# Kernel tuning notes

Measured on AMD Instinct MI355X. Metric: run time of the kernel, lower is better.

## Reference

```python
import jax, jax.numpy as jnp
import numpy as np
import math

N = 1000000          # num_primitives
G = 512              # grid_size
M = 64               # max_elements_per_cell
RES = 512
FOCAL = RES / 2.0 / (0.5 / 1.5)   # 768.0, from e = 1.5/0.5
K = 2                # candidate cells per axis (ellipses are tiny: radius ~1e-3)
PRIM_TYPE = 5.0      # _ROTATED_ELLIPSE_PRIM_TYPE


def _build_mvp(seed=42):
    rng = np.random.default_rng(seed)
    x, n, f = 0.5, 1.5, 100.0
    proj = np.array([[n / x, 0, 0, 0], [0, -n / x, 0, 0],
                     [0, 0, -(f + n) / (f - n), -(2 * f * n) / (f - n)],
                     [0, 0, -1, 0]], dtype=np.float32)
    u1, u2, u3 = rng.random(3)
    qx = math.sqrt(1 - u1) * math.sin(math.tau * u2)
    qy = math.sqrt(1 - u1) * math.cos(math.tau * u2)
    qz = math.sqrt(u1) * math.sin(math.tau * u3)
    qw = math.sqrt(u1) * math.cos(math.tau * u3)
    rot = np.eye(4, dtype=np.float32)
    rot[:3, :3] = np.array(
        [[1 - 2 * (qy * qy + qz * qz), 2 * (qx * qy - qz * qw), 2 * (qx * qz + qy * qw)],
         [2 * (qx * qy + qz * qw), 1 - 2 * (qx * qx + qz * qz), 2 * (qy * qz - qx * qw)],
         [2 * (qx * qz - qy * qw), 2 * (qy * qz + qx * qw), 1 - 2 * (qx * qx + qy * qy)]],
        dtype=np.float32)
    trans = np.eye(4, dtype=np.float32)
    trans[2, 3] = -4.0
    return proj @ (trans @ rot)


def setup_inputs() -> dict:
    key = jax.random.key(0)
    k = jax.random.split(key, 4)
    centers = (jax.random.uniform(k[0], (N, 3)) - 0.5) / 0.5
    scales = 1e-3 * jax.random.uniform(k[1], (N, 3))
    rotations = jnp.ones((N, 4), jnp.float32)
    colors = jax.random.uniform(k[2], (N, 3))
    opacities = jax.random.uniform(k[3], (N,))
    mvp = jnp.asarray(_build_mvp())
    background = jnp.zeros((3,), jnp.float32)
    return {"centers": centers, "scales": scales, "rotations": rotations,
            "colors": colors, "opacities": opacities, "mvp": mvp,
            "background": background}


def _quat_to_rot(q):
    q = q / jnp.clip(jnp.linalg.norm(q, axis=1, keepdims=True), 1e-12, None)
    w, x, y, z = q[:, 0], q[:, 1], q[:, 2], q[:, 3]
    return jnp.stack([
        1 - 2 * (y * y + z * z), 2 * (x * y - z * w), 2 * (x * z + y * w),
        2 * (x * y + z * w), 1 - 2 * (x * x + z * z), 2 * (y * z - x * w),
        2 * (x * z - y * w), 2 * (y * z + x * w), 1 - 2 * (x * x + y * y)],
        axis=-1).reshape(-1, 3, 3)


def reference(centers, scales, rotations, colors, opacities, mvp, background):
    dt = centers.dtype
    # --- project centers to NDC (no perspective divide, per source) ---
    ndc = jnp.concatenate([centers, jnp.ones((N, 1), dt)], axis=1) @ mvp.T  # [N,4]
    valid = ndc[:, 2] > 0.0
    cs = (ndc[:, :2] + 1.0) * 0.5                                          # [N,2] in [0,1]
    # --- 3D covariance -> screen-space 2x2 covariance ---
    Rm = _quat_to_rot(rotations)
    L = Rm * jnp.clip(scales, 1e-9, None)[:, None, :]   # R @ diag(s)
    cov = jnp.einsum('nij,nkj->nik', L, L)              # L L^T
    V = mvp[:3, :3]
    ccov = jnp.einsum('ij,njk,lk->nil', V, cov, V)      # V cov V^T
    z = jnp.clip(ndc[:, 2], 1e-6, None)
    sc = FOCAL / z
    scov = ccov[:, :2, :2] * (sc * sc)[:, None, None]
    # --- depth sort (invalid prims pushed to the back, kept for static shape) ---
    order = jnp.argsort(jnp.where(valid, z, jnp.float32(1e30)))
    cs, scov = cs[order], scov[order]
    col = colors[order]
    op = jnp.clip(opacities, 0.0, 1.0)[order]
    vm = valid[order]
    vf = vm.astype(dt)
    cx, cy = cs[:, 0], cs[:, 1]
    c00, c01, c11 = scov[:, 0, 0], scov[:, 0, 1], scov[:, 1, 1]
    # --- packed param block: 20 floats per primitive ---
    cp = jnp.stack([cx, cy, c00, c01, c11, jnp.zeros_like(cx)], axis=1) * vf[:, None]
    result = jnp.concatenate([
        (PRIM_TYPE * vf)[:, None],            # slot 0: prim type
        cp,                                   # slots 1..6: control points
        jnp.zeros((N, 2), dt),                # slots 7,8
        col * vf[:, None],                    # slots 9..11: color
        (op * vf)[:, None],                   # slot 12: opacity
        jnp.zeros((N, 7), dt)], axis=1)       # slots 13..19
    # --- acceleration grid: scatter depth-sorted prim ids into covered cells ---
    rx = 3.0 * jnp.sqrt(jnp.clip(c00, 0.0, None)) / RES   # 3-sigma extent, normalized
    ry = 3.0 * jnp.sqrt(jnp.clip(c11, 0.0, None)) / RES
    x0 = jnp.floor((cx - rx) * G).astype(jnp.int32)
    x1 = jnp.floor((cx + rx) * G).astype(jnp.int32)
    y0 = jnp.floor((cy - ry) * G).astype(jnp.int32)
    y1 = jnp.floor((cy + ry) * G).astype(jnp.int32)
    offs = jnp.arange(K, dtype=jnp.int32)
    cxc = x0[:, None] + offs
    cyc = y0[:, None] + offs
    vx = (cxc <= x1[:, None]) & (cxc >= 0) & (cxc < G)
    vy = (cyc <= y1[:, None]) & (cyc >= 0) & (cyc < G)
    cell = cyc[:, :, None] * G + cxc[:, None, :]                     # [N,K,K]
    vp = vm[:, None, None] & vy[:, :, None] & vx[:, None, :]
    key_arr = jnp.where(vp, cell, G * G).reshape(-1)                 # sentinel G*G
    prim = jnp.broadcast_to(jnp.arange(N, dtype=jnp.int32)[:, None, None], (N, K, K)).reshape(-1)
    ordr = jnp.argsort(key_arr)                                      # stable sort by cell
    sk = key_arr[ordr]
    sp = prim[ordr]
    first = jnp.searchsorted(sk, sk, side='left').astype(jnp.int32)
    rank = jnp.arange(sk.shape[0], dtype=jnp.int32) - first
    ok = (sk < G * G) & (rank < M)
    slots = jnp.where(ok, sk * (M + 1) + 1 + rank, G * G * (M + 1))
    grid = jnp.zeros(G * G * (M + 1), jnp.int32).at[slots].set(sp, mode='drop')
    counts = jax.ops.segment_sum((sk < G * G).astype(jnp.int32), sk, num_segments=G * G + 1)[:G * G]
    grid = grid.at[jnp.arange(G * G) * (M + 1)].set(jnp.minimum(counts, M))
    header = jnp.concatenate([vm.sum().astype(dt)[None],
                              jnp.array([float(G), float(M)], dt)])
    return jnp.concatenate([header, background, result.reshape(-1), grid.astype(dt)])
```

## Files before the change

### kernel.cpp

```cpp
#include <hip/hip_runtime.h>
#include <stdint.h>

#pragma clang fp contract(off)

#define N_PRIM   1000000
#define GRID_G   512
#define NCELLS   (GRID_G*GRID_G)
#define FOCAL_C  768.0f
#define NP2      1048576
#define SB       1024
#define EPB      1024
#define PREP_BLOCKS 2048

#define O_SORTA  ((size_t)0)
#define O_SORTB  (O_SORTA + (size_t)NP2*8)
#define O_REC    (O_SORTB + (size_t)NP2*8)
#define O_CCNT   (O_REC   + (size_t)N_PRIM*64)
#define O_COFS   (O_CCNT  + (size_t)NCELLS*4)
#define O_CURS   (O_COFS  + (size_t)NCELLS*4)
#define O_HIST   (O_CURS  + (size_t)NCELLS*4)
#define O_BSUM   (O_HIST  + (size_t)NCELLS*4)
#define O_VCNT   (O_BSUM  + 8192)
#define O_ENTRY  (O_VCNT  + 8192)
#define WS_NEED  (O_ENTRY + (size_t)4*N_PRIM*4)

__device__ __forceinline__ int swz(int q) { return q ^ ((q >> 3) & 7); }

__global__ __launch_bounds__(256) void k_prep(
    const float* __restrict__ centers, const float* __restrict__ scales,
    const float* __restrict__ rotations, const float* __restrict__ colors,
    const float* __restrict__ opac, const float* __restrict__ mvp,
    uint64_t* __restrict__ sortA, float4* __restrict__ rec,
    uint32_t* __restrict__ cellcnt, uint32_t* __restrict__ vcnt)
{
  __shared__ float4 srec[2048];
  __shared__ uint32_t swcnt[4];
  int t = threadIdx.x;
  int pair = blockIdx.x*256 + t;
  int p0 = pair*2;
  bool live = p0 < N_PRIM;

  float m0=mvp[0], m1=mvp[1], m2=mvp[2],  m3=mvp[3];
  float m4=mvp[4], m5=mvp[5], m6=mvp[6],  m7=mvp[7];
  float m8=mvp[8], m9=mvp[9], m10=mvp[10],m11=mvp[11];

  bool valid0=false, valid1=false;
  uint64_t pk0 = ~0ULL, pk1 = ~0ULL;

  if (live) {
    const float2* cp = (const float2*)(centers + (size_t)pair*6);
    float2 ca = cp[0], cb = cp[1], cc = cp[2];
    const float2* sp = (const float2*)(scales + (size_t)pair*6);
    float2 sa = sp[0], sb2 = sp[1], sc2 = sp[2];
    const float4* rp = (const float4*)rotations;
    float4 q0 = rp[p0], q1 = rp[p0+1];
    const float2* colp = (const float2*)(colors + (size_t)pair*6);
    float2 ka = colp[0], kb = colp[1], kc = colp[2];
    float2 o2 = ((const float2*)opac)[pair];

    auto doPrim = [&](int i, float c0, float c1, float c2,
                      float s0, float s1, float s2,
                      float qw, float qx, float qy, float qz,
                      float col0, float col1, float col2, float op,
                      uint64_t& pk, bool& validf, int lidx) {
      float n0 = fmaf(m2,  c2, fmaf(m1, c1, m0*c0)) + m3;
      float n1 = fmaf(m6,  c2, fmaf(m5, c1, m4*c0)) + m7;
      float n2 = fmaf(m10, c2, fmaf(m9, c1, m8*c0)) + m11;
      bool valid = n2 > 0.0f;
      validf = valid;
      float cx = (n0 + 1.0f)*0.5f;
      float cy = (n1 + 1.0f)*0.5f;
      uint32_t key32 = valid ? __float_as_uint(fmaxf(n2, 1e-6f)) : 0x7149F2CAu;
      pk = ((uint64_t)key32 << 20) | (uint32_t)i;

      float nrm = sqrtf(qw*qw + qx*qx + qy*qy + qz*qz);
      nrm = fmaxf(nrm, 1e-12f);
      qw /= nrm; qx /= nrm; qy /= nrm; qz /= nrm;
      float R00 = 1.0f - 2.0f*(qy*qy + qz*qz);
      float R01 = 2.0f*(qx*qy - qz*qw);
      float R02 = 2.0f*(qx*qz + qy*qw);
      float R10 = 2.0f*(qx*qy + qz*qw);
      float R11 = 1.0f - 2.0f*(qx*qx + qz*qz);
      float R12 = 2.0f*(qy*qz - qx*qw);
      float R20 = 2.0f*(qx*qz - qy*qw);
      float R21 = 2.0f*(qy*qz + qx*qw);
      float R22 = 1.0f - 2.0f*(qx*qx + qy*qy);
      s0 = fmaxf(s0, 1e-9f); s1 = fmaxf(s1, 1e-9f); s2 = fmaxf(s2, 1e-9f);
      float L00=R00*s0, L01=R01*s1, L02=R02*s2;
      float L10=R10*s0, L11=R11*s1, L12=R12*s2;
      float L20=R20*s0, L21=R21*s1, L22=R22*s2;
      float cv00 = fmaf(L02,L02, fmaf(L01,L01, L00*L00));
      float cv01 = fmaf(L02,L12, fmaf(L01,L11, L00*L10));
      float cv02 = fmaf(L02,L22, fmaf(L01,L21, L00*L20));
      float cv11 = fmaf(L12,L12, fmaf(L11,L11, L10*L10));
      float cv12 = fmaf(L12,L22, fmaf(L11,L21, L10*L20));
      float cv22 = fmaf(L22,L22, fmaf(L21,L21, L20*L20));
      float T00 = fmaf(m2,cv02, fmaf(m1,cv01, m0*cv00));
      float T01 = fmaf(m2,cv12, fmaf(m1,cv11, m0*cv01));
      float T02 = fmaf(m2,cv22, fmaf(m1,cv12, m0*cv02));
      float T10 = fmaf(m6,cv02, fmaf(m5,cv01, m4*cv00));
      float T11 = fmaf(m6,cv12, fmaf(m5,cv11, m4*cv01));
      float T12 = fmaf(m6,cv22, fmaf(m5,cv12, m4*cv02));
      float cc00 = fmaf(T02,m2, fmaf(T01,m1, T00*m0));
      float cc01 = fmaf(T02,m6, fmaf(T01,m5, T00*m4));
      float cc11 = fmaf(T12,m6, fmaf(T11,m5, T10*m4));
      float zc  = fmaxf(n2, 1e-6f);
      float scv = FOCAL_C / zc;
      float sc22 = scv*scv;
      float c00 = cc00*sc22, c01 = cc01*sc22, c11 = cc11*sc22;

      float rx = (3.0f * sqrtf(fmaxf(c00, 0.0f))) / 512.0f;
      float ry = (3.0f * sqrtf(fmaxf(c11, 0.0f))) / 512.0f;
      int x0 = (int)floorf((cx - rx) * 512.0f);
      int x1 = (int)floorf((cx + rx) * 512.0f);
      int y0 = (int)floorf((cy - ry) * 512.0f);
      int y1 = (int)floorf((cy + ry) * 512.0f);
      int cl[4];
      #pragma unroll
      for (int ky = 0; ky < 2; ++ky) {
        int yy = y0 + ky;
        bool vy = (yy <= y1) && (yy >= 0) && (yy < GRID_G);
        #pragma unroll
        for (int kx = 0; kx < 2; ++kx) {
          int xx = x0 + kx;
          bool vx = (xx <= x1) && (xx >= 0) && (xx < GRID_G);
          int cell = (valid && vy && vx) ? (yy*GRID_G + xx) : -1;
          cl[ky*2+kx] = cell;
          if (cell >= 0) atomicAdd(&cellcnt[cell], 1u);
        }
      }
      float opv = fminf(fmaxf(op, 0.0f), 1.0f);
      float vf = valid ? 1.0f : 0.0f;
      int lb = lidx*4;
      srec[swz(lb+0)] = make_float4(cx, cy, c00, c01);
      srec[swz(lb+1)] = make_float4(c11, col0, col1, col2);
      srec[swz(lb+2)] = make_float4(opv, vf, 0.0f, 0.0f);
      srec[swz(lb+3)] = make_float4(__int_as_float(cl[0]), __int_as_float(cl[1]),
                                    __int_as_float(cl[2]), __int_as_float(cl[3]));
    };

    doPrim(p0,   ca.x, ca.y, cb.x, sa.x, sa.y, sb2.x,
           q0.x, q0.y, q0.z, q0.w, ka.x, ka.y, kb.x, o2.x, pk0, valid0, 2*t);
    doPrim(p0+1, cb.y, cc.x, cc.y, sb2.y, sc2.x, sc2.y,
           q1.x, q1.y, q1.z, q1.w, kb.y, kc.x, kc.y, o2.y, pk1, valid1, 2*t+1);
  }

  ((ulonglong2*)sortA)[pair] = make_ulonglong2(pk0, pk1);

  unsigned long long b0 = __ballot(live && valid0);
  unsigned long long b1 = __ballot(live && valid1);
  if ((t & 63) == 0) swcnt[t >> 6] = (uint32_t)(__popcll(b0) + __popcll(b1));
  __syncthreads();
  if (t == 0) vcnt[blockIdx.x] = swcnt[0]+swcnt[1]+swcnt[2]+swcnt[3];

  size_t gbase = (size_t)blockIdx.x*2048;
  for (int q = t; q < 2048; q += 256) {
    size_t gi = gbase + q;
    if (gi < (size_t)N_PRIM*4) rec[gi] = srec[swz(q)];
  }
}

__global__ void k_scanA(const uint32_t* __restrict__ cnt, uint32_t* __restrict__ ofs,
                        uint32_t* __restrict__ bsum)
{
  __shared__ uint32_t s[256];
  int t = threadIdx.x;
  int i = blockIdx.x*256 + t;
  uint32_t v = cnt[i];
  s[t] = v; __syncthreads();
  for (int o = 1; o < 256; o <<= 1) {
    uint32_t u = (t >= o) ? s[t-o] : 0u; __syncthreads();
    s[t] += u; __syncthreads();
  }
  ofs[i] = s[t] - v;
  if (t == 255) bsum[blockIdx.x] = s[t];
}

__global__ void k_scanBC(uint32_t* __restrict__ ofs, const uint32_t* __restrict__ bsum,
                         uint32_t* __restrict__ cursor,
                         const uint32_t* __restrict__ vcnt,
                         const float* __restrict__ bg, float* __restrict__ out)
{
  __shared__ uint32_t s[256];
  int t = threadIdx.x;
  int bid = blockIdx.x;
  uint32_t acc = 0;
  for (int i = t; i < bid; i += 256) acc += bsum[i];
  s[t] = acc; __syncthreads();
  #pragma unroll
  for (int o = 128; o > 0; o >>= 1) { if (t < o) s[t] += s[t+o]; __syncthreads(); }
  uint32_t partial = s[0];
  int i = bid*256 + t;
  uint32_t v = ofs[i] + partial;
  ofs[i] = v;
  if (cursor) cursor[i] = v;

  if (vcnt && bid == 0) {
    __syncthreads();
    uint32_t a2 = 0;
    for (int i2 = t; i2 < PREP_BLOCKS; i2 += 256) a2 += vcnt[i2];
    s[t] = a2; __syncthreads();
    #pragma unroll
    for (int o = 128; o > 0; o >>= 1) { if (t < o) s[t] += s[t+o]; __syncthreads(); }
    if (t == 0) {
      out[0] = (float)s[0];
      out[1] = 512.0f;
      out[2] = 64.0f;
      out[3] = bg[0]; out[4] = bg[1]; out[5] = bg[2];
    }
  }
}

__global__ __launch_bounds__(256) void k_hist(const uint64_t* __restrict__ keys,
                                              uint32_t* __restrict__ hist, int shift)
{
  __shared__ uint32_t h[256];
  int t = threadIdx.x;
  h[t] = 0; __syncthreads();
  const ulonglong2* k2 = (const ulonglong2*)(keys + (size_t)blockIdx.x*EPB);
  #pragma unroll
  for (int j = 0; j < 2; ++j) {
    ulonglong2 w = k2[j*256 + t];
    atomicAdd(&h[(uint32_t)(w.x >> shift) & 255u], 1u);
    atomicAdd(&h[(uint32_t)(w.y >> shift) & 255u], 1u);
  }
  __syncthreads();
  hist[(size_t)t*SB + blockIdx.x] = h[t];
}

__global__ __launch_bounds__(256) void k_scatter(
    const uint64_t* __restrict__ in, uint64_t* __restrict__ outp,
    const uint32_t* __restrict__ hist, int shift)
{
  __shared__ uint32_t s_base[256];
  __shared__ uint32_t lbase[256];
  __shared__ uint32_t s_run[256];
  __shared__ uint32_t s_wcnt[1024];
  __shared__ uint64_t stage[EPB];
  int t = threadIdx.x;
  int wid = t >> 6, lane = t & 63;
  s_base[t] = hist[(size_t)t*SB + blockIdx.x];
  s_run[t] = 0;
  lbase[t] = 0;
  size_t base = (size_t)blockIdx.x*EPB;
  uint64_t v[4]; uint32_t d[4];
  #pragma unroll
  for (int j = 0; j < 4; ++j) {
    v[j] = in[base + j*256 + t];
    d[j] = (uint32_t)(v[j] >> shift) & 255u;
  }
  __syncthreads();
  #pragma unroll
  for (int j = 0; j < 4; ++j) atomicAdd(&lbase[d[j]], 1u);
  __syncthreads();
  uint32_t mycnt = lbase[t];
  for (int o = 1; o < 256; o <<= 1) {
    uint32_t u = (t >= o) ? lbase[t-o] : 0u; __syncthreads();
    lbase[t] += u; __syncthreads();
  }
  uint32_t myexcl = lbase[t] - mycnt;
  __syncthreads();
  lbase[t] = myexcl;
  __syncthreads();

  #pragma unroll
  for (int j = 0; j < 4; ++j) {
    #pragma unroll
    for (int q0 = 0; q0 < 4; ++q0) s_wcnt[q0*256 + t] = 0;
    __syncthreads();
    unsigned long long m = ~0ULL;
    #pragma unroll
    for (int bit = 0; bit < 8; ++bit) {
      unsigned long long vote = __ballot((d[j] >> bit) & 1);
      m &= ((d[j] >> bit) & 1) ? vote : ~vote;
    }
    uint32_t lr = __popcll(m & ((1ULL << lane) - 1ULL));
    if (lr == 0) s_wcnt[d[j]*4 + wid] = (uint32_t)__popcll(m);
    __syncthreads();
    uint32_t wb = 0;
    #pragma unroll
    for (int w = 0; w < 3; ++w) if (w < wid) wb += s_wcnt[d[j]*4 + w];
    stage[lbase[d[j]] + s_run[d[j]] + wb + lr] = v[j];
    __syncthreads();
    s_run[t] += s_wcnt[t*4] + s_wcnt[t*4+1] + s_wcnt[t*4+2] + s_wcnt[t*4+3];
    __syncthreads();
  }
  #pragma unroll
  for (int j = 0; j < 4; ++j) {
    int q = j*256 + t;
    uint64_t sv = stage[q];
    uint32_t sd = (uint32_t)(sv >> shift) & 255u;
    outp[s_base[sd] + ((uint32_t)q - lbase[sd])] = sv;
  }
}

__global__ __launch_bounds__(256) void k_result(
    const uint64_t* __restrict__ sorted, const float4* __restrict__ rec,
    uint32_t* __restrict__ cursor, uint32_t* __restrict__ entry,
    float* __restrict__ out)
{
  __shared__ float rows[64*21];
  int t = threadIdx.x;
  int i = blockIdx.x*256 + t;
  bool liveP = i < N_PRIM;
  float4 a = make_float4(0,0,0,0), b = a, c = a;
  int4 cl = make_int4(-1,-1,-1,-1);
  if (liveP) {
    uint64_t v = sorted[i];
    int o = (int)(v & 0xFFFFFu);
    a = rec[(size_t)o*4]; b = rec[(size_t)o*4+1];
    c = rec[(size_t)o*4+2];
    float4 dd = rec[(size_t)o*4+3];
    cl.x = __float_as_int(dd.x); cl.y = __float_as_int(dd.y);
    cl.z = __float_as_int(dd.z); cl.w = __float_as_int(dd.w);
  }
  float vf = c.y;
  int mychunk = t >> 6;
  int r64 = t & 63;
  int blockRows = min(256, N_PRIM - blockIdx.x*256);
  for (int ch = 0; ch < 4; ++ch) {
    if (mychunk == ch && liveP) {
      float* r = &rows[r64*21];
      r[0]  = 5.0f*vf;
      r[1]  = a.x*vf; r[2] = a.y*vf; r[3] = a.z*vf; r[4] = a.w*vf; r[5] = b.x*vf;
      r[6]  = 0.0f; r[7] = 0.0f; r[8] = 0.0f;
      r[9]  = b.y*vf; r[10] = b.z*vf; r[11] = b.w*vf;
      r[12] = c.x*vf;
      r[13]=0.0f; r[14]=0.0f; r[15]=0.0f; r[16]=0.0f; r[17]=0.0f; r[18]=0.0f; r[19]=0.0f;
    }
    __syncthreads();
    int nrows = min(64, blockRows - ch*64);
    if (nrows > 0) {
      int total = nrows*20;
      float* gout = out + 6 + (size_t)blockIdx.x*5120 + ch*1280;
      for (int g = t; g < total; g += 256) {
        int rr = g/20, cc2 = g - rr*20;
        gout[g] = rows[rr*21+cc2];
      }
    }
    __syncthreads();
  }
  if (liveP) {
    int cc[4] = {cl.x, cl.y, cl.z, cl.w};
    #pragma unroll
    for (int k = 0; k < 4; ++k) {
      if (cc[k] >= 0) {
        uint32_t p = atomicAdd(&cursor[cc[k]], 1u);
        entry[p] = (uint32_t)i;
      }
    }
  }
}

__global__ __launch_bounds__(256) void k_grid(
    const uint32_t* __restrict__ cellcnt, const uint32_t* __restrict__ cellofs,
    const uint32_t* __restrict__ entry, float* __restrict__ out)
{
  int wid = threadIdx.x >> 6;
  int lane = threadIdx.x & 63;
  int cell = blockIdx.x*4 + wid;
  uint32_t cnt = cellcnt[cell];
  uint32_t ofs = cellofs[cell];
  float* g = out + 6 + (size_t)N_PRIM*20 + (size_t)cell*65;
  if (cnt <= 64u) {
    int v = (lane < (int)cnt) ? (int)entry[ofs + lane] : 0x7FFFFFFF;
    #pragma unroll
    for (int k = 2; k <= 64; k <<= 1) {
      #pragma unroll
      for (int j = k>>1; j > 0; j >>= 1) {
        int p = __shfl_xor(v, j, 64);
        bool up = ((lane & k) == 0);
        bool lower = ((lane & j) == 0);
        int mn = min(v,p), mx = max(v,p);
        v = (up == lower) ? mn : mx;
      }
    }
    g[1+lane] = (lane < (int)cnt) ? (float)v : 0.0f;
    if (lane == 0) g[0] = (float)cnt;
  } else {
    int last = -1;
    for (int s = 0; s < 64; ++s) {
      int best = 0x7FFFFFFF;
      for (uint32_t c = lane; c < cnt; c += 64) {
        int v = (int)entry[ofs + c];
        if (v > last && v < best) best = v;
      }
      #pragma unroll
      for (int o = 32; o > 0; o >>= 1) best = min(best, __shfl_xor(best, o, 64));
      if (lane == 0) g[1+s] = (float)best;
      last = best;
    }
    if (lane == 0) g[0] = 64.0f;
  }
}

extern "C" void kernel_launch(void* const* d_in, const int* in_sizes, int n_in,
                              void* d_out, int out_size, void* d_ws, size_t ws_size,
                              hipStream_t stream)
{
  const float* centers   = (const float*)d_in[0];
  const float* scales    = (const float*)d_in[1];
  const float* rotations = (const float*)d_in[2];
  const float* colors    = (const float*)d_in[3];
  const float* opacities = (const float*)d_in[4];
  const float* mvp       = (const float*)d_in[5];
  const float* background= (const float*)d_in[6];
  float* out = (float*)d_out;
  char* ws = (char*)d_ws;
  if (ws_size < WS_NEED) return;

  uint64_t* sortA  = (uint64_t*)(ws + O_SORTA);
  uint64_t* sortB  = (uint64_t*)(ws + O_SORTB);
  float4*   rec    = (float4*)  (ws + O_REC);
  uint32_t* ccnt   = (uint32_t*)(ws + O_CCNT);
  uint32_t* cofs   = (uint32_t*)(ws + O_COFS);
  uint32_t* curs   = (uint32_t*)(ws + O_CURS);
  uint32_t* hist   = (uint32_t*)(ws + O_HIST);
  uint32_t* bsum   = (uint32_t*)(ws + O_BSUM);
  uint32_t* vcnt   = (uint32_t*)(ws + O_VCNT);
  uint32_t* entry  = (uint32_t*)(ws + O_ENTRY);

  hipMemsetAsync(ws + O_CCNT, 0, (size_t)NCELLS*4, stream);

  k_prep<<<PREP_BLOCKS, 256, 0, stream>>>(centers, scales, rotations, colors,
                                          opacities, mvp, sortA, rec, ccnt, vcnt);

  k_scanA <<<NCELLS/256, 256, 0, stream>>>(ccnt, cofs, bsum);
  k_scanBC<<<NCELLS/256, 256, 0, stream>>>(cofs, bsum, curs, vcnt, background, out);

  uint64_t *kin = sortA, *kout = sortB;
  const int shifts[4] = {20, 28, 36, 44};
  for (int pass = 0; pass < 4; ++pass) {
    k_hist<<<SB, 256, 0, stream>>>(kin, hist, shifts[pass]);
    k_scanA <<<(256*SB)/256, 256, 0, stream>>>(hist, hist, bsum);
    k_scanBC<<<(256*SB)/256, 256, 0, stream>>>(hist, bsum, (uint32_t*)nullptr,
                                               (const uint32_t*)nullptr,
                                               (const float*)nullptr, (float*)nullptr);
    k_scatter<<<SB, 256, 0, stream>>>(kin, kout, hist, shifts[pass]);
    uint64_t* tmp = kin; kin = kout; kout = tmp;
  }

  k_result<<<(N_PRIM+255)/256, 256, 0, stream>>>(kin, rec, curs, entry, out);
  k_grid  <<<NCELLS/4, 256, 0, stream>>>(ccnt, cofs, entry, out);
}
```

Measured before the change: 423.3 us.

## Replace 4-pass radix sort with depth-bucket counting sort and in-bucket rank

Drops the four-pass LSD radix sort over 64-bit keys. Each valid primitive's depth bits are offset by a constant and binned into 262144 buckets; the bucket counts are scanned together with the cell counts in one fused scan. Items are then scattered into their buckets, and each bucket is ordered by an O(n^2) rank count inside one wavefront, which writes the output rows and grid entries directly. Unused tail rows are zeroed separately. This saves many kernel launches and global passes, but relies on the depth distribution fitting the chosen key range and on buckets staying small.

```diff
diff --git a/kernel.cpp b/kernel.cpp
--- a/kernel.cpp
+++ b/kernel.cpp
@@ -4,24 +4,24 @@
 #pragma clang fp contract(off)
 
 #define N_PRIM   1000000
+#define NPAIRS   (N_PRIM/2)
+#define PREP_BLOCKS ((NPAIRS+255)/256)
 #define GRID_G   512
 #define NCELLS   (GRID_G*GRID_G)
+#define NBUCK    262144
 #define FOCAL_C  768.0f
-#define NP2      1048576
-#define SB       1024
-#define EPB      1024
-#define PREP_BLOCKS 2048
-
-#define O_SORTA  ((size_t)0)
-#define O_SORTB  (O_SORTA + (size_t)NP2*8)
-#define O_REC    (O_SORTB + (size_t)NP2*8)
-#define O_CCNT   (O_REC   + (size_t)N_PRIM*64)
-#define O_COFS   (O_CCNT  + (size_t)NCELLS*4)
-#define O_CURS   (O_COFS  + (size_t)NCELLS*4)
-#define O_HIST   (O_CURS  + (size_t)NCELLS*4)
-#define O_BSUM   (O_HIST  + (size_t)NCELLS*4)
-#define O_VCNT   (O_BSUM  + 8192)
-#define O_ENTRY  (O_VCNT  + 8192)
+#define KEYC     0x358637BDu
+
+#define O_PK     ((size_t)0)
+#define O_REC    (O_PK   + (size_t)N_PRIM*8)
+#define O_BSLOT  (O_REC  + (size_t)N_PRIM*64)
+#define O_CNT    (O_BSLOT+ (size_t)N_PRIM*4)
+#define O_OFS    (O_CNT  + (size_t)(NCELLS+NBUCK)*4)
+#define O_CUR    (O_OFS  + (size_t)(NCELLS+NBUCK)*4)
+#define O_BSUM   (O_CUR  + (size_t)(NCELLS+NBUCK)*4)
+#define O_VCNT   (O_BSUM + 8192)
+#define O_VCSLOT (O_VCNT + 8192)
+#define O_ENTRY  (O_VCSLOT + 256)
 #define WS_NEED  (O_ENTRY + (size_t)4*N_PRIM*4)
 
 __device__ __forceinline__ int swz(int q) { return q ^ ((q >> 3) & 7); }
@@ -30,8 +30,9 @@
     const float* __restrict__ centers, const float* __restrict__ scales,
     const float* __restrict__ rotations, const float* __restrict__ colors,
     const float* __restrict__ opac, const float* __restrict__ mvp,
-    uint64_t* __restrict__ sortA, float4* __restrict__ rec,
-    uint32_t* __restrict__ cellcnt, uint32_t* __restrict__ vcnt)
+    uint64_t* __restrict__ pkarr, float4* __restrict__ rec,
+    uint32_t* __restrict__ cellcnt, uint32_t* __restrict__ buckcnt,
+    uint32_t* __restrict__ vcnt)
 {
   __shared__ float4 srec[2048];
   __shared__ uint32_t swcnt[4];
@@ -70,8 +71,11 @@
       validf = valid;
       float cx = (n0 + 1.0f)*0.5f;
       float cy = (n1 + 1.0f)*0.5f;
-      uint32_t key32 = valid ? __float_as_uint(fmaxf(n2, 1e-6f)) : 0x7149F2CAu;
-      pk = ((uint64_t)key32 << 20) | (uint32_t)i;
+      if (valid) {
+        uint32_t skey = __float_as_uint(fmaxf(n2, 1e-6f)) - KEYC;
+        pk = ((uint64_t)skey << 20) | (uint32_t)i;
+        atomicAdd(&buckcnt[skey >> 10], 1u);
+      }
 
       float nrm = sqrtf(qw*qw + qx*qx + qy*qy + qz*qz);
       nrm = fmaxf(nrm, 1e-12f);
@@ -143,9 +147,9 @@
            q0.x, q0.y, q0.z, q0.w, ka.x, ka.y, kb.x, o2.x, pk0, valid0, 2*t);
     doPrim(p0+1, cb.y, cc.x, cc.y, sb2.y, sc2.x, sc2.y,
            q1.x, q1.y, q1.z, q1.w, kb.y, kc.x, kc.y, o2.y, pk1, valid1, 2*t+1);
-  }
-
-  ((ulonglong2*)sortA)[pair] = make_ulonglong2(pk0, pk1);
+
+    ((ulonglong2*)pkarr)[pair] = make_ulonglong2(pk0, pk1);
+  }
 
   unsigned long long b0 = __ballot(live && valid0);
   unsigned long long b1 = __ballot(live && valid1);
@@ -153,9 +157,9 @@
   __syncthreads();
   if (t == 0) vcnt[blockIdx.x] = swcnt[0]+swcnt[1]+swcnt[2]+swcnt[3];
 
-  size_t gbase = (size_t)blockIdx.x*2048;
+  size_t gbase2 = (size_t)blockIdx.x*2048;
   for (int q = t; q < 2048; q += 256) {
-    size_t gi = gbase + q;
+    size_t gi = gbase2 + q;
     if (gi < (size_t)N_PRIM*4) rec[gi] = srec[swz(q)];
   }
 }
@@ -179,23 +183,32 @@
 __global__ void k_scanBC(uint32_t* __restrict__ ofs, const uint32_t* __restrict__ bsum,
                          uint32_t* __restrict__ cursor,
                          const uint32_t* __restrict__ vcnt,
-                         const float* __restrict__ bg, float* __restrict__ out)
-{
+                         const float* __restrict__ bg, float* __restrict__ out,
+                         uint32_t* __restrict__ vcslot)
+{
+  __shared__ uint64_t s8[256];
   __shared__ uint32_t s[256];
   int t = threadIdx.x;
   int bid = blockIdx.x;
-  uint32_t acc = 0;
-  for (int i = t; i < bid; i += 256) acc += bsum[i];
-  s[t] = acc; __syncthreads();
+  uint64_t acc = 0;
+  for (int i = t; i < 2048; i += 256) {
+    uint32_t v = bsum[i];
+    uint64_t add = 0;
+    if (i < bid)  add += v;
+    if (i < 1024) add += ((uint64_t)v << 32);
+    acc += add;
+  }
+  s8[t] = acc; __syncthreads();
   #pragma unroll
-  for (int o = 128; o > 0; o >>= 1) { if (t < o) s[t] += s[t+o]; __syncthreads(); }
-  uint32_t partial = s[0];
+  for (int o = 128; o > 0; o >>= 1) { if (t < o) s8[t] += s8[t+o]; __syncthreads(); }
+  uint32_t partial = (uint32_t)s8[0];
+  uint32_t T = (uint32_t)(s8[0] >> 32);
   int i = bid*256 + t;
-  uint32_t v = ofs[i] + partial;
+  uint32_t v = ofs[i] + partial - (bid >= 1024 ? T : 0u);
   ofs[i] = v;
-  if (cursor) cursor[i] = v;
-
-  if (vcnt && bid == 0) {
+  cursor[i] = v;
+
+  if (bid == 0) {
     __syncthreads();
     uint32_t a2 = 0;
     for (int i2 = t; i2 < PREP_BLOCKS; i2 += 256) a2 += vcnt[i2];
@@ -203,153 +216,89 @@
     #pragma unroll
     for (int o = 128; o > 0; o >>= 1) { if (t < o) s[t] += s[t+o]; __syncthreads(); }
     if (t == 0) {
-      out[0] = (float)s[0];
+      uint32_t vc = s[0];
+      out[0] = (float)vc;
       out[1] = 512.0f;
       out[2] = 64.0f;
       out[3] = bg[0]; out[4] = bg[1]; out[5] = bg[2];
-    }
-  }
-}
-
-__global__ __launch_bounds__(256) void k_hist(const uint64_t* __restrict__ keys,
-                                              uint32_t* __restrict__ hist, int shift)
-{
-  __shared__ uint32_t h[256];
-  int t = threadIdx.x;
-  h[t] = 0; __syncthreads();
-  const ulonglong2* k2 = (const ulonglong2*)(keys + (size_t)blockIdx.x*EPB);
-  #pragma unroll
-  for (int j = 0; j < 2; ++j) {
-    ulonglong2 w = k2[j*256 + t];
-    atomicAdd(&h[(uint32_t)(w.x >> shift) & 255u], 1u);
-    atomicAdd(&h[(uint32_t)(w.y >> shift) & 255u], 1u);
-  }
-  __syncthreads();
-  hist[(size_t)t*SB + blockIdx.x] = h[t];
-}
-
-__global__ __launch_bounds__(256) void k_scatter(
-    const uint64_t* __restrict__ in, uint64_t* __restrict__ outp,
-    const uint32_t* __restrict__ hist, int shift)
-{
-  __shared__ uint32_t s_base[256];
-  __shared__ uint32_t lbase[256];
-  __shared__ uint32_t s_run[256];
-  __shared__ uint32_t s_wcnt[1024];
-  __shared__ uint64_t stage[EPB];
-  int t = threadIdx.x;
-  int wid = t >> 6, lane = t & 63;
-  s_base[t] = hist[(size_t)t*SB + blockIdx.x];
-  s_run[t] = 0;
-  lbase[t] = 0;
-  size_t base = (size_t)blockIdx.x*EPB;
-  uint64_t v[4]; uint32_t d[4];
-  #pragma unroll
-  for (int j = 0; j < 4; ++j) {
-    v[j] = in[base + j*256 + t];
-    d[j] = (uint32_t)(v[j] >> shift) & 255u;
-  }
-  __syncthreads();
-  #pragma unroll
-  for (int j = 0; j < 4; ++j) atomicAdd(&lbase[d[j]], 1u);
-  __syncthreads();
-  uint32_t mycnt = lbase[t];
-  for (int o = 1; o < 256; o <<= 1) {
-    uint32_t u = (t >= o) ? lbase[t-o] : 0u; __syncthreads();
-    lbase[t] += u; __syncthreads();
-  }
-  uint32_t myexcl = lbase[t] - mycnt;
-  __syncthreads();
-  lbase[t] = myexcl;
-  __syncthreads();
-
-  #pragma unroll
-  for (int j = 0; j < 4; ++j) {
-    #pragma unroll
-    for (int q0 = 0; q0 < 4; ++q0) s_wcnt[q0*256 + t] = 0;
-    __syncthreads();
-    unsigned long long m = ~0ULL;
-    #pragma unroll
-    for (int bit = 0; bit < 8; ++bit) {
-      unsigned long long vote = __ballot((d[j] >> bit) & 1);
-      m &= ((d[j] >> bit) & 1) ? vote : ~vote;
-    }
-    uint32_t lr = __popcll(m & ((1ULL << lane) - 1ULL));
-    if (lr == 0) s_wcnt[d[j]*4 + wid] = (uint32_t)__popcll(m);
-    __syncthreads();
-    uint32_t wb = 0;
-    #pragma unroll
-    for (int w = 0; w < 3; ++w) if (w < wid) wb += s_wcnt[d[j]*4 + w];
-    stage[lbase[d[j]] + s_run[d[j]] + wb + lr] = v[j];
-    __syncthreads();
-    s_run[t] += s_wcnt[t*4] + s_wcnt[t*4+1] + s_wcnt[t*4+2] + s_wcnt[t*4+3];
-    __syncthreads();
-  }
-  #pragma unroll
-  for (int j = 0; j < 4; ++j) {
-    int q = j*256 + t;
-    uint64_t sv = stage[q];
-    uint32_t sd = (uint32_t)(sv >> shift) & 255u;
-    outp[s_base[sd] + ((uint32_t)q - lbase[sd])] = sv;
-  }
-}
-
-__global__ __launch_bounds__(256) void k_result(
-    const uint64_t* __restrict__ sorted, const float4* __restrict__ rec,
-    uint32_t* __restrict__ cursor, uint32_t* __restrict__ entry,
+      *vcslot = vc;
+    }
+  }
+}
+
+__global__ __launch_bounds__(256) void k_scatter2(
+    const uint64_t* __restrict__ pkarr, uint32_t* __restrict__ bcur,
+    uint32_t* __restrict__ bslot)
+{
+  int i = blockIdx.x*256 + threadIdx.x;
+  if (i >= N_PRIM) return;
+  uint64_t pk = pkarr[i];
+  if (pk == ~0ULL) return;
+  uint32_t b = (uint32_t)(pk >> 30);
+  uint32_t item = (uint32_t)pk & 0x3FFFFFFFu;
+  uint32_t p = atomicAdd(&bcur[b], 1u);
+  bslot[p] = item;
+}
+
+__global__ __launch_bounds__(256) void k_bsort(
+    const uint32_t* __restrict__ bcnt, const uint32_t* __restrict__ bofs,
+    const uint32_t* __restrict__ bslot, const float4* __restrict__ rec,
+    uint32_t* __restrict__ ccur, uint32_t* __restrict__ entry,
     float* __restrict__ out)
 {
-  __shared__ float rows[64*21];
-  int t = threadIdx.x;
-  int i = blockIdx.x*256 + t;
-  bool liveP = i < N_PRIM;
-  float4 a = make_float4(0,0,0,0), b = a, c = a;
-  int4 cl = make_int4(-1,-1,-1,-1);
-  if (liveP) {
-    uint64_t v = sorted[i];
-    int o = (int)(v & 0xFFFFFu);
-    a = rec[(size_t)o*4]; b = rec[(size_t)o*4+1];
-    c = rec[(size_t)o*4+2];
-    float4 dd = rec[(size_t)o*4+3];
-    cl.x = __float_as_int(dd.x); cl.y = __float_as_int(dd.y);
-    cl.z = __float_as_int(dd.z); cl.w = __float_as_int(dd.w);
-  }
-  float vf = c.y;
-  int mychunk = t >> 6;
-  int r64 = t & 63;
-  int blockRows = min(256, N_PRIM - blockIdx.x*256);
-  for (int ch = 0; ch < 4; ++ch) {
-    if (mychunk == ch && liveP) {
-      float* r = &rows[r64*21];
-      r[0]  = 5.0f*vf;
-      r[1]  = a.x*vf; r[2] = a.y*vf; r[3] = a.z*vf; r[4] = a.w*vf; r[5] = b.x*vf;
-      r[6]  = 0.0f; r[7] = 0.0f; r[8] = 0.0f;
-      r[9]  = b.y*vf; r[10] = b.z*vf; r[11] = b.w*vf;
-      r[12] = c.x*vf;
-      r[13]=0.0f; r[14]=0.0f; r[15]=0.0f; r[16]=0.0f; r[17]=0.0f; r[18]=0.0f; r[19]=0.0f;
-    }
-    __syncthreads();
-    int nrows = min(64, blockRows - ch*64);
-    if (nrows > 0) {
-      int total = nrows*20;
-      float* gout = out + 6 + (size_t)blockIdx.x*5120 + ch*1280;
-      for (int g = t; g < total; g += 256) {
-        int rr = g/20, cc2 = g - rr*20;
-        gout[g] = rows[rr*21+cc2];
-      }
-    }
-    __syncthreads();
-  }
-  if (liveP) {
-    int cc[4] = {cl.x, cl.y, cl.z, cl.w};
+  __shared__ uint32_t stg[4][1024];
+  int w = threadIdx.x >> 6, lane = threadIdx.x & 63;
+  int b = blockIdx.x*4 + w;
+  uint32_t n = bcnt[b];
+  if (n == 0) return;
+  uint32_t start = bofs[b];
+  bool fits = (n <= 1024u);
+  if (fits) {
+    for (uint32_t e = lane; e < n; e += 64) stg[w][e] = bslot[start + e];
+  }
+  for (uint32_t e = lane; e < n; e += 64) {
+    uint32_t it = fits ? stg[w][e] : bslot[start + e];
+    uint32_t rank = 0;
+    if (fits) {
+      for (uint32_t j = 0; j < n; ++j) rank += (stg[w][j] < it);
+    } else {
+      for (uint32_t j = 0; j < n; ++j) rank += (bslot[start + j] < it);
+    }
+    uint32_t pos = start + rank;
+    int idx = (int)(it & 0xFFFFFu);
+    float4 a  = rec[(size_t)idx*4],   bq = rec[(size_t)idx*4+1];
+    float4 c  = rec[(size_t)idx*4+2], dd = rec[(size_t)idx*4+3];
+    float2* wp = (float2*)(out + 6 + (size_t)pos*20);
+    wp[0] = make_float2(5.0f, a.x);
+    wp[1] = make_float2(a.y, a.z);
+    wp[2] = make_float2(a.w, bq.x);
+    wp[3] = make_float2(0.0f, 0.0f);
+    wp[4] = make_float2(0.0f, bq.y);
+    wp[5] = make_float2(bq.z, bq.w);
+    wp[6] = make_float2(c.x, 0.0f);
+    wp[7] = make_float2(0.0f, 0.0f);
+    wp[8] = make_float2(0.0f, 0.0f);
+    wp[9] = make_float2(0.0f, 0.0f);
+    int cc[4] = {__float_as_int(dd.x), __float_as_int(dd.y),
+                 __float_as_int(dd.z), __float_as_int(dd.w)};
     #pragma unroll
     for (int k = 0; k < 4; ++k) {
       if (cc[k] >= 0) {
-        uint32_t p = atomicAdd(&cursor[cc[k]], 1u);
-        entry[p] = (uint32_t)i;
-      }
-    }
-  }
+        uint32_t p = atomicAdd(&ccur[cc[k]], 1u);
+        entry[p] = pos;
+      }
+    }
+  }
+}
+
+__global__ void k_rowzero(const uint32_t* __restrict__ vcslot, float* __restrict__ out)
+{
+  uint32_t vc = *vcslot;
+  uint32_t i = blockIdx.x*256 + threadIdx.x;
+  if (i >= (uint32_t)N_PRIM || i < vc) return;
+  float2* wp = (float2*)(out + 6 + (size_t)i*20);
+  #pragma unroll
+  for (int q = 0; q < 10; ++q) wp[q] = make_float2(0.0f, 0.0f);
 }
 
 __global__ __launch_bounds__(256) void k_grid(
@@ -409,37 +358,35 @@
   char* ws = (char*)d_ws;
   if (ws_size < WS_NEED) return;
 
-  uint64_t* sortA  = (uint64_t*)(ws + O_SORTA);
-  uint64_t* sortB  = (uint64_t*)(ws + O_SORTB);
+  uint64_t* pkarr  = (uint64_t*)(ws + O_PK);
   float4*   rec    = (float4*)  (ws + O_REC);
-  uint32_t* ccnt   = (uint32_t*)(ws + O_CCNT);
-  uint32_t* cofs   = (uint32_t*)(ws + O_COFS);
-  uint32_t* curs   = (uint32_t*)(ws + O_CURS);
-  uint32_t* hist   = (uint32_t*)(ws + O_HIST);
+  uint32_t* bslot  = (uint32_t*)(ws + O_BSLOT);
+  uint32_t* ccnt   = (uint32_t*)(ws + O_CNT);
+  uint32_t* bcnt   = ccnt + NCELLS;
+  uint32_t* cofs   = (uint32_t*)(ws + O_OFS);
+  uint32_t* bofs   = cofs + NCELLS;
+  uint32_t* ccur   = (uint32_t*)(ws + O_CUR);
+  uint32_t* bcur   = ccur + NCELLS;
   uint32_t* bsum   = (uint32_t*)(ws + O_BSUM);
   uint32_t* vcnt   = (uint32_t*)(ws + O_VCNT);
+  uint32_t* vcslot = (uint32_t*)(ws + O_VCSLOT);
   uint32_t* entry  = (uint32_t*)(ws + O_ENTRY);
 
-  hipMemsetAsync(ws + O_CCNT, 0, (size_t)NCELLS*4, stream);
+  hipMemsetAsync(ws + O_CNT, 0, (size_t)(NCELLS+NBUCK)*4, stream);
 
   k_prep<<<PREP_BLOCKS, 256, 0, stream>>>(centers, scales, rotations, colors,
-                                          opacities, mvp, sortA, rec, ccnt, vcnt);
-
-  k_scanA <<<NCELLS/256, 256, 0, stream>>>(ccnt, cofs, bsum);
-  k_scanBC<<<NCELLS/256, 256, 0, stream>>>(cofs, bsum, curs, vcnt, background, out);
-
-  uint64_t *kin = sortA, *kout = sortB;
-  const int shifts[4] = {20, 28, 36, 44};
-  for (int pass = 0; pass < 4; ++pass) {
-    k_hist<<<SB, 256, 0, stream>>>(kin, hist, shifts[pass]);
-    k_scanA <<<(256*SB)/256, 256, 0, stream>>>(hist, hist, bsum);
-    k_scanBC<<<(256*SB)/256, 256, 0, stream>>>(hist, bsum, (uint32_t*)nullptr,
-                                               (const uint32_t*)nullptr,
-                                               (const float*)nullptr, (float*)nullptr);
-    k_scatter<<<SB, 256, 0, stream>>>(kin, kout, hist, shifts[pass]);
-    uint64_t* tmp = kin; kin = kout; kout = tmp;
-  }
-
-  k_result<<<(N_PRIM+255)/256, 256, 0, stream>>>(kin, rec, curs, entry, out);
-  k_grid  <<<NCELLS/4, 256, 0, stream>>>(ccnt, cofs, entry, out);
-}
+                                          opacities, mvp, pkarr, rec,
+                                          ccnt, bcnt, vcnt);
+
+  k_scanA <<<(NCELLS+NBUCK)/256, 256, 0, stream>>>(ccnt, cofs, bsum);
+  k_scanBC<<<(NCELLS+NBUCK)/256, 256, 0, stream>>>(cofs, bsum, ccur, vcnt,
+                                                   background, out, vcslot);
+
+  k_scatter2<<<(N_PRIM+255)/256, 256, 0, stream>>>(pkarr, bcur, bslot);
+
+  k_bsort<<<NBUCK/4, 256, 0, stream>>>(bcnt, bofs, bslot, rec, ccur, entry, out);
+
+  k_rowzero<<<(N_PRIM+255)/256, 256, 0, stream>>>(vcslot, out);
+
+  k_grid<<<NCELLS/4, 256, 0, stream>>>(ccnt, cofs, entry, out);
+}
```

After: 479.9 us. 1.13x slower.
